# Performance work log

Measured on AMD Instinct MI355X. Metric: run time of the kernel, lower is better.

The kernel has to match this reference:

```python
import jax, jax.numpy as jnp
import numpy as np

V = 32000   # vocab
T = 256     # context len
C = 384     # n_embed
H = 6       # heads
D = 64      # head dim (HEAD_SIZE // NUM_HEADS)
L = 6       # blocks
B = 16      # batch
FF = 4 * C


def setup_inputs() -> dict:
    key = jax.random.key(0)
    ks = jax.random.split(key, 16)
    s = 0.02
    p = {}
    p["x_ids"] = jax.random.randint(ks[0], (B, T), 0, V)
    p["y_ids"] = jax.random.randint(ks[1], (B, T), 0, V)
    p["tok_emb"] = jax.random.normal(ks[2], (V, C), jnp.float32) * s
    p["pos_emb"] = jax.random.normal(ks[3], (T, C), jnp.float32) * s
    p["Wq"] = jax.random.normal(ks[4], (L, H, C, D), jnp.float32) * s
    p["Wk"] = jax.random.normal(ks[5], (L, H, C, D), jnp.float32) * s
    p["Wv"] = jax.random.normal(ks[6], (L, H, C, D), jnp.float32) * s
    p["Wo"] = jax.random.normal(ks[7], (L, H * D, C), jnp.float32) * s
    p["bo"] = jnp.zeros((L, C), jnp.float32)
    p["ln1_s"] = jnp.ones((L, C), jnp.float32)
    p["ln1_b"] = jnp.zeros((L, C), jnp.float32)
    p["ln2_s"] = jnp.ones((L, C), jnp.float32)
    p["ln2_b"] = jnp.zeros((L, C), jnp.float32)
    p["W1"] = jax.random.normal(ks[8], (L, C, FF), jnp.float32) * s
    p["b1"] = jnp.zeros((L, FF), jnp.float32)
    p["W2"] = jax.random.normal(ks[9], (L, FF, C), jnp.float32) * s
    p["b2"] = jnp.zeros((L, C), jnp.float32)
    p["lnf_s"] = jnp.ones((C,), jnp.float32)
    p["lnf_b"] = jnp.zeros((C,), jnp.float32)
    p["Whead"] = jax.random.normal(ks[10], (C, V), jnp.float32) * s
    p["bhead"] = jnp.zeros((V,), jnp.float32)
    return p


def _ln(x, scale, bias, eps=1e-5):
    m = x.mean(-1, keepdims=True)
    v = ((x - m) ** 2).mean(-1, keepdims=True)
    return (x - m) * jax.lax.rsqrt(v + eps) * scale + bias


def reference(x_ids, y_ids, tok_emb, pos_emb, Wq, Wk, Wv, Wo, bo,
              ln1_s, ln1_b, ln2_s, ln2_b, W1, b1, W2, b2,
              lnf_s, lnf_b, Whead, bhead):
    Bq, Tq = x_ids.shape
    x = tok_emb[x_ids] + pos_emb[:Tq]                      # [B,T,C]
    mask = jnp.tril(jnp.ones((Tq, Tq), bool))
    scale = C ** -0.5  # NOTE: original scales by input dim C, not head dim
    for l in range(L):
        h = _ln(x, ln1_s[l], ln1_b[l])
        q = jnp.einsum('btc,hcd->bhtd', h, Wq[l])
        k = jnp.einsum('btc,hcd->bhtd', h, Wk[l])
        v = jnp.einsum('btc,hcd->bhtd', h, Wv[l])
        att = jnp.einsum('bhtd,bhsd->bhts', q, k) * scale
        att = jnp.where(mask, att, -jnp.inf)
        att = jax.nn.softmax(att, axis=-1)
        o = jnp.einsum('bhts,bhsd->bhtd', att, v)
        o = o.transpose(0, 2, 1, 3).reshape(Bq, Tq, H * D)  # concat heads
        x = x + o @ Wo[l] + bo[l]
        h2 = _ln(x, ln2_s[l], ln2_b[l])
        x = x + jax.nn.relu(h2 @ W1[l] + b1[l]) @ W2[l] + b2[l]
    x = _ln(x, lnf_s, lnf_b)
    logits = x @ Whead + bhead                             # [B,T,V]
    logp = jax.nn.log_softmax(logits, axis=-1)
    loss = -jnp.take_along_axis(logp, y_ids[..., None], axis=-1).mean()
    return (logits, loss)
```

## Files before the change

kernel.cpp:

```cpp
#include <hip/hip_runtime.h>

typedef unsigned short u16;
typedef u16   u16x8 __attribute__((ext_vector_type(8)));
typedef short s16x8 __attribute__((ext_vector_type(8)));
typedef float f32x4 __attribute__((ext_vector_type(4)));

#define NV 32000
#define NT 256
#define NC 384
#define NH 6
#define ND 64
#define NL 6
#define NB 16
#define NFF 1536
#define NM (NB*NT)
#define QKVSZ (NB*NH*NT*ND)
#define NSLAB (NV/64)

__device__ __forceinline__ u16 f2bf(float f){
    unsigned x = __builtin_bit_cast(unsigned, f);
    x += 0x7fffu + ((x>>16)&1u);
    return (u16)(x>>16);
}

__device__ __forceinline__ void gload_lds16(const u16* g, u16* l){
    __builtin_amdgcn_global_load_lds((const __attribute__((address_space(1))) unsigned int*)g,
                                     (__attribute__((address_space(3))) unsigned int*)l, 16, 0, 0);
}

__global__ __launch_bounds__(256) void embed_kernel(const int* __restrict__ ids,
        const float* __restrict__ tok, const float* __restrict__ pos, float* __restrict__ x){
    int i4 = (blockIdx.x*256 + threadIdx.x)*4;
    int m = i4 / NC; int c = i4 - m*NC; int t = m & (NT-1);
    const float4 a = *(const float4*)(tok + (size_t)ids[m]*NC + c);
    const float4 b = *(const float4*)(pos + t*NC + c);
    *(float4*)(x + i4) = float4{a.x+b.x, a.y+b.y, a.z+b.z, a.w+b.w};
}

__global__ __launch_bounds__(256) void ln_kernel(const float* __restrict__ x,
        const float* __restrict__ sc, const float* __restrict__ bi, u16* __restrict__ out){
    int row  = blockIdx.x*4 + (threadIdx.x>>6);
    int lane = threadIdx.x & 63;
    const float* xr = x + (size_t)row*NC;
    float v[6]; float sum = 0.f, sq = 0.f;
    #pragma unroll
    for (int i=0;i<6;++i){ v[i]=xr[lane+64*i]; sum+=v[i]; sq+=v[i]*v[i]; }
    #pragma unroll
    for (int off=1; off<64; off<<=1){ sum += __shfl_xor(sum,off); sq += __shfl_xor(sq,off); }
    float mean = sum*(1.f/NC);
    float var  = sq*(1.f/NC) - mean*mean;
    float rstd = rsqrtf(var + 1e-5f);
    u16* orow = out + (size_t)row*NC;
    #pragma unroll
    for (int i=0;i<6;++i){ int c = lane+64*i; orow[c] = f2bf((v[i]-mean)*rstd*sc[c] + bi[c]); }
}

struct TDesc {
    const float* in; u16* out;
    int Cc; int nx; int perZ; int obDiv; int oStride; int start;
    long inBatch; long oS1; long oS2; float scale;
};
struct TPack { TDesc d[7]; };

__global__ __launch_bounds__(256) void tconv_all(TPack p){
    __shared__ float tile[32][33];
    int bid = blockIdx.x;
    int e = 0;
    #pragma unroll
    for (int i=1;i<7;++i) e += (bid >= p.d[i].start) ? 1 : 0;
    TDesc D = p.d[e];
    int local = bid - D.start;
    int bz  = local / D.perZ; int rem = local - bz*D.perZ;
    int cy  = rem / D.nx;     int cx  = rem - cy*D.nx;
    int r0 = cy*32, c0 = cx*32;
    const float* ib = D.in + (size_t)bz*D.inBatch;
    u16* ob = D.out + (size_t)(bz/D.obDiv)*D.oS1 + (size_t)(bz%D.obDiv)*D.oS2;
    int tx = threadIdx.x & 31, ty = threadIdx.x >> 5;
    #pragma unroll
    for (int i=0;i<4;++i) tile[ty+8*i][tx] = ib[(size_t)(r0+ty+8*i)*D.Cc + (c0+tx)];
    __syncthreads();
    #pragma unroll
    for (int i=0;i<4;++i) ob[(size_t)(c0+ty+8*i)*D.oStride + (r0+tx)] = f2bf(tile[tx][ty+8*i]*D.scale);
}

template<int EPI, int BM>
__global__ __launch_bounds__(256,2) void gemm_bt(
        const u16* __restrict__ A, const u16* __restrict__ Bt,
        const float* __restrict__ bias, float* __restrict__ resid,
        u16* __restrict__ outb, float* __restrict__ outf, float* __restrict__ lpart,
        int M, int N, int K){
    constexpr int MI = BM/32;
    __shared__ u16 As[BM*32];
    __shared__ u16 Bs[128*32];
    int tid = threadIdx.x;
    int lane = tid & 63, wid = tid >> 6;
    int wm = wid >> 1, wn = wid & 1;
    int l15 = lane & 15, lg = lane >> 4;
    int m0 = blockIdx.y * BM, n0 = blockIdx.x * 128;
    f32x4 acc[MI][4];
    #pragma unroll
    for (int a=0;a<MI;++a)
        #pragma unroll
        for (int b=0;b<4;++b) acc[a][b] = f32x4{0.f,0.f,0.f,0.f};

    int nk = K >> 5;
    for (int kk = 0; kk < nk; ++kk){
        int k0 = kk << 5;
        #pragma unroll
        for (int i=0;i<BM/64;++i){
            int o   = i*4096 + tid*16;
            int row = o >> 6;
            int kb  = (o & 63) >> 1;
            gload_lds16(A + (size_t)(m0+row)*K + (k0+kb), As + (o>>1));
        }
        #pragma unroll
        for (int i=0;i<2;++i){
            int o   = i*4096 + tid*16;
            int row = o >> 6;
            int kb  = (o & 63) >> 1;
            gload_lds16(Bt + (size_t)(n0+row)*K + (k0+kb), Bs + (o>>1));
        }
        asm volatile("s_waitcnt vmcnt(0)" ::: "memory");
        __syncthreads();
        s16x8 af[MI], bfr[4];
        #pragma unroll
        for (int mi=0;mi<MI;++mi) af[mi]  = *(const s16x8*)&As[(wm*(BM/2)+mi*16+l15)*32 + lg*8];
        #pragma unroll
        for (int ni=0;ni<4;++ni) bfr[ni] = *(const s16x8*)&Bs[(wn*64+ni*16+l15)*32 + lg*8];
        #pragma unroll
        for (int mi=0;mi<MI;++mi)
            #pragma unroll
            for (int ni=0;ni<4;++ni)
                acc[mi][ni] = __builtin_amdgcn_mfma_f32_16x16x32_bf16(af[mi], bfr[ni], acc[mi][ni], 0,0,0);
        __syncthreads();
    }

    if (EPI == 3){
        float es[MI][4];
        #pragma unroll
        for (int mi=0;mi<MI;++mi)
            #pragma unroll
            for (int r=0;r<4;++r) es[mi][r] = 0.f;
        #pragma unroll
        for (int mi=0;mi<MI;++mi)
            #pragma unroll
            for (int ni=0;ni<4;++ni)
                #pragma unroll
                for (int r=0;r<4;++r){
                    int mg = m0 + wm*(BM/2) + mi*16 + lg*4 + r;
                    int ng = n0 + wn*64 + ni*16 + l15;
                    float val = acc[mi][ni][r] + bias[ng];
                    outf[(size_t)mg*N + ng] = val;
                    es[mi][r] += __expf(val);
                }
        #pragma unroll
        for (int mi=0;mi<MI;++mi)
            #pragma unroll
            for (int r=0;r<4;++r){
                float s = es[mi][r];
                s += __shfl_xor(s,1); s += __shfl_xor(s,2);
                s += __shfl_xor(s,4); s += __shfl_xor(s,8);
                if (l15 == 0){
                    int mg = m0 + wm*(BM/2) + mi*16 + lg*4 + r;
                    lpart[(size_t)mg*NSLAB + blockIdx.x*2 + wn] = s;
                }
            }
        return;
    }

    #pragma unroll
    for (int mi=0;mi<MI;++mi){
        #pragma unroll
        for (int ni=0;ni<4;++ni){
            #pragma unroll
            for (int r=0;r<4;++r){
                int mg = m0 + wm*(BM/2) + mi*16 + lg*4 + r;
                int ng = n0 + wn*64 + ni*16 + l15;
                float c = acc[mi][ni][r];
                if (EPI == 0){
                    int which = ng / NC; int hd = ng - which*NC;
                    int hh = hd >> 6, d = hd & 63;
                    int bb = mg >> 8, tt = mg & (NT-1);
                    outb[(size_t)which*QKVSZ + ((size_t)(bb*NH+hh)*NT + tt)*ND + d] = f2bf(c);
                } else if (EPI == 1){
                    float* pp = resid + (size_t)mg*N + ng;
                    *pp = *pp + c + bias[ng];
                } else if (EPI == 2){
                    outb[(size_t)mg*N + ng] = f2bf(fmaxf(c + bias[ng], 0.f));
                }
            }
        }
    }
}

__global__ __launch_bounds__(256,2) void attn_kernel(const u16* __restrict__ qkv, u16* __restrict__ o){
    int blk = blockIdx.x;
    int qt = blk & 3, bh = blk >> 2;
    int b = bh / NH, h = bh - b*NH;
    int tid = threadIdx.x, lane = tid & 63, w = tid >> 6;
    int l15 = lane & 15, lg = lane >> 4;
    __shared__ u16 Ks[256*72];
    __shared__ u16 Vt[64*264];
    __shared__ u16 Ps[4][16*72];
    const u16* qb = qkv + (size_t)bh*NT*ND;
    const u16* kb = qb + QKVSZ;
    const u16* vb = kb + QKVSZ;
    int nit = (qt+1)*2;
    for (int it=0; it<nit; ++it){
        int idx = it*256 + tid;
        int e0 = idx*8;
        int row = e0 >> 6, col = e0 & 63;
        *(u16x8*)&Ks[row*72+col] = *(const u16x8*)(kb + e0);
        u16x8 vv = *(const u16x8*)(vb + e0);
        #pragma unroll
        for (int j=0;j<8;++j) Vt[(col+j)*264 + row] = vv[j];
    }
    const u16* qrow = qb + (size_t)(qt*64 + w*16 + l15)*ND;
    s16x8 qf[2];
    qf[0] = *(const s16x8*)(qrow + lg*8);
    qf[1] = *(const s16x8*)(qrow + 32 + lg*8);
    __syncthreads();

    f32x4 oacc[4]; float l_[4];
    #pragma unroll
    for (int c=0;c<4;++c){ oacc[c]=f32x4{0.f,0.f,0.f,0.f}; l_[c]=0.f; }
    u16* Pw = &Ps[w][0];

    for (int kt=0; kt<=qt; ++kt){
        f32x4 sacc[4];
        #pragma unroll
        for (int c=0;c<4;++c) sacc[c]=f32x4{0.f,0.f,0.f,0.f};
        #pragma unroll
        for (int ks=0;ks<2;++ks){
            s16x8 kf[4];
            #pragma unroll
            for (int ni=0;ni<4;++ni)
                kf[ni] = *(const s16x8*)&Ks[(kt*64+ni*16+l15)*72 + ks*32 + lg*8];
            #pragma unroll
            for (int ni=0;ni<4;++ni)
                sacc[ni] = __builtin_amdgcn_mfma_f32_16x16x32_bf16(qf[ks], kf[ni], sacc[ni], 0,0,0);
        }
        if (kt == qt){
            #pragma unroll
            for (int ni=0;ni<4;++ni)
                #pragma unroll
                for (int r=0;r<4;++r)
                    if (ni*16+l15 > w*16+lg*4+r) sacc[ni][r] = -1e30f;
        }
        #pragma unroll
        for (int r=0;r<4;++r){
            float rs = 0.f;
            #pragma unroll
            for (int ni=0;ni<4;++ni){
                float p = __expf(sacc[ni][r]);
                sacc[ni][r] = p;
                rs += p;
                Pw[(lg*4+r)*72 + ni*16 + l15] = f2bf(p);
            }
            rs += __shfl_xor(rs,1); rs += __shfl_xor(rs,2);
            rs += __shfl_xor(rs,4); rs += __shfl_xor(rs,8);
            l_[r] += rs;
        }
        #pragma unroll
        for (int ks=0;ks<2;++ks){
            s16x8 pf, vf[4];
            pf = *(const s16x8*)&Pw[l15*72 + ks*32 + lg*8];
            #pragma unroll
            for (int ni=0;ni<4;++ni)
                vf[ni] = *(const s16x8*)&Vt[(ni*16+l15)*264 + kt*64 + ks*32 + lg*8];
            #pragma unroll
            for (int ni=0;ni<4;++ni)
                oacc[ni] = __builtin_amdgcn_mfma_f32_16x16x32_bf16(pf, vf[ni], oacc[ni], 0,0,0);
        }
    }
    #pragma unroll
    for (int ni=0;ni<4;++ni)
        #pragma unroll
        for (int r=0;r<4;++r){
            int t = qt*64 + w*16 + lg*4 + r;
            int d = ni*16 + l15;
            o[((size_t)(b*NT + t))*NC + h*ND + d] = f2bf(oacc[ni][r] / l_[r]);
        }
}

__global__ __launch_bounds__(256) void loss_rows2(const float* __restrict__ lpart,
        const float* __restrict__ logits, const int* __restrict__ y, float* __restrict__ rowloss){
    int row  = blockIdx.x*4 + (threadIdx.x>>6);
    int lane = threadIdx.x & 63;
    const float* pr = lpart + (size_t)row*NSLAB;
    float s = 0.f;
    for (int i = lane; i < NSLAB; i += 64) s += pr[i];
    #pragma unroll
    for (int off=1; off<64; off<<=1) s += __shfl_xor(s, off);
    if (lane==0)
        rowloss[row] = logf(s) - logits[(size_t)row*NV + y[row]];
}

__global__ __launch_bounds__(256) void loss_final(const float* __restrict__ rowloss, float* __restrict__ out){
    int tid = threadIdx.x;
    float s = 0.f;
    for (int i = tid; i < NM; i += 256) s += rowloss[i];
    #pragma unroll
    for (int off=1; off<64; off<<=1) s += __shfl_xor(s, off);
    __shared__ float ss[4];
    if ((tid&63)==0) ss[tid>>6]=s;
    __syncthreads();
    if (tid==0) out[0] = (ss[0]+ss[1]+ss[2]+ss[3]) * (1.f/NM);
}

extern "C" void kernel_launch(void* const* d_in, const int* in_sizes, int n_in,
                              void* d_out, int out_size, void* d_ws, size_t ws_size,
                              hipStream_t stream){
    const int*   x_ids = (const int*)  d_in[0];
    const int*   y_ids = (const int*)  d_in[1];
    const float* tok   = (const float*)d_in[2];
    const float* pos   = (const float*)d_in[3];
    const float* Wq    = (const float*)d_in[4];
    const float* Wk    = (const float*)d_in[5];
    const float* Wv    = (const float*)d_in[6];
    const float* Wo    = (const float*)d_in[7];
    const float* bo    = (const float*)d_in[8];
    const float* ln1s  = (const float*)d_in[9];
    const float* ln1b  = (const float*)d_in[10];
    const float* ln2s  = (const float*)d_in[11];
    const float* ln2b  = (const float*)d_in[12];
    const float* W1    = (const float*)d_in[13];
    const float* b1    = (const float*)d_in[14];
    const float* W2    = (const float*)d_in[15];
    const float* b2    = (const float*)d_in[16];
    const float* lnfs  = (const float*)d_in[17];
    const float* lnfb  = (const float*)d_in[18];
    const float* Wh    = (const float*)d_in[19];
    const float* bh    = (const float*)d_in[20];

    float* logits = (float*)d_out;
    float* lossp  = logits + (size_t)NM*NV;

    char* ws = (char*)d_ws;
    auto alloc = [&](size_t bytes)->char*{ char* p = ws; ws += (bytes + 255) & ~(size_t)255; return p; };
    float* xf    = (float*)alloc((size_t)NM*NC*4);
    u16*   hbf   = (u16*)  alloc((size_t)NM*NC*2);
    u16*   qkvb  = (u16*)  alloc((size_t)3*QKVSZ*2);
    u16*   obf   = (u16*)  alloc((size_t)NM*NC*2);
    u16*   f1bf  = (u16*)  alloc((size_t)NM*NFF*2);
    u16*   qkvw  = (u16*)  alloc((size_t)NL*1152*NC*2);
    u16*   wot   = (u16*)  alloc((size_t)NL*NC*NC*2);
    u16*   w1t   = (u16*)  alloc((size_t)NL*NFF*NC*2);
    u16*   w2t   = (u16*)  alloc((size_t)NL*NC*NFF*2);
    u16*   wht   = (u16*)  alloc((size_t)NV*NC*2);
    float* part  = (float*)alloc((size_t)NM*4);
    float* lpart = (float*)qkvb;

    const float qscale = 0.051031036307982884f;

    TPack tp;
    tp.d[0] = {Wq, qkvw + 0*(NC*NC), ND,  2,  24, NH, NC, 0,     (long)NC*ND, (long)1152*NC, (long)ND*NC, qscale};
    tp.d[1] = {Wk, qkvw + 1*(NC*NC), ND,  2,  24, NH, NC, 864,   (long)NC*ND, (long)1152*NC, (long)ND*NC, 1.f};
    tp.d[2] = {Wv, qkvw + 2*(NC*NC), ND,  2,  24, NH, NC, 1728,  (long)NC*ND, (long)1152*NC, (long)ND*NC, 1.f};
    tp.d[3] = {Wo, wot,              NC, 12, 144, 1,  NC, 2592,  (long)NC*NC, (long)NC*NC,   0,           1.f};
    tp.d[4] = {W1, w1t,             NFF, 48, 576, 1,  NC, 3456,  (long)NC*NFF,(long)NFF*NC,  0,           1.f};
    tp.d[5] = {W2, w2t,              NC, 12, 576, 1, NFF, 6912,  (long)NFF*NC,(long)NC*NFF,  0,           1.f};
    tp.d[6] = {Wh, wht,              NV,1000,12000,1, NC, 10368, 0,           0,             0,           1.f};
    tconv_all<<<22368,256,0,stream>>>(tp);

    embed_kernel<<<NM*NC/1024,256,0,stream>>>(x_ids, tok, pos, xf);
    for (int l = 0; l < NL; ++l){
        ln_kernel<<<NM/4,256,0,stream>>>(xf, ln1s + l*NC, ln1b + l*NC, hbf);
        gemm_bt<0,64><<<dim3(1152/128, NM/64),256,0,stream>>>(hbf, qkvw + (size_t)l*1152*NC,
                nullptr, nullptr, qkvb, nullptr, nullptr, NM, 1152, NC);
        attn_kernel<<<NB*NH*4,256,0,stream>>>(qkvb, obf);
        gemm_bt<1,64><<<dim3(NC/128, NM/64),256,0,stream>>>(obf, wot + (size_t)l*NC*NC,
                bo + l*NC, xf, nullptr, nullptr, nullptr, NM, NC, NC);
        ln_kernel<<<NM/4,256,0,stream>>>(xf, ln2s + l*NC, ln2b + l*NC, hbf);
        gemm_bt<2,64><<<dim3(NFF/128, NM/64),256,0,stream>>>(hbf, w1t + (size_t)l*NFF*NC,
                b1 + l*NFF, nullptr, f1bf, nullptr, nullptr, NM, NFF, NC);
        gemm_bt<1,64><<<dim3(NC/128, NM/64),256,0,stream>>>(f1bf, w2t + (size_t)l*NC*NFF,
                b2 + l*NC, xf, nullptr, nullptr, nullptr, NM, NC, NFF);
    }
    ln_kernel<<<NM/4,256,0,stream>>>(xf, lnfs, lnfb, hbf);
    gemm_bt<3,128><<<dim3(NV/128, NM/128),256,0,stream>>>(hbf, wht, bh,
            nullptr, nullptr, logits, lpart, NM, NV, NC);
    loss_rows2<<<NM/4,256,0,stream>>>(lpart, logits, y_ids, part);
    loss_final<<<1,256,0,stream>>>(part, lossp);
}
```

Baseline: 836.4 us.

## Widen GEMM K-step, enlarge LM-head tile with grid swizzle, fuse embed with LN

The GEMM template gains a BN parameter and loads a K-step of 64, split into two 32-wide LDS halves, so each loop iteration runs twice as many MFMAs per barrier pair. The LM-head GEMM moves to 128x256 tiles, with a block-index swizzle that groups blocks sharing the same vocab slab to improve L2 reuse of the head weights, and NSLAB is halved to match. The embedding kernel is fused with the first layernorm, which removes one full pass over the activations. The costs are more LDS per block, which may lower occupancy, more accumulator registers in the 128x256 head GEMM, and a swizzle that hardcodes 32 M-tiles.

```diff
diff --git a/kernel.cpp b/kernel.cpp
--- a/kernel.cpp
+++ b/kernel.cpp
@@ -15,7 +15,7 @@
 #define NFF 1536
 #define NM (NB*NT)
 #define QKVSZ (NB*NH*NT*ND)
-#define NSLAB (NV/64)
+#define NSLAB (NV/128)
 
 __device__ __forceinline__ u16 f2bf(float f){
     unsigned x = __builtin_bit_cast(unsigned, f);
@@ -28,13 +28,31 @@
                                      (__attribute__((address_space(3))) unsigned int*)l, 16, 0, 0);
 }
 
-__global__ __launch_bounds__(256) void embed_kernel(const int* __restrict__ ids,
-        const float* __restrict__ tok, const float* __restrict__ pos, float* __restrict__ x){
-    int i4 = (blockIdx.x*256 + threadIdx.x)*4;
-    int m = i4 / NC; int c = i4 - m*NC; int t = m & (NT-1);
-    const float4 a = *(const float4*)(tok + (size_t)ids[m]*NC + c);
-    const float4 b = *(const float4*)(pos + t*NC + c);
-    *(float4*)(x + i4) = float4{a.x+b.x, a.y+b.y, a.z+b.z, a.w+b.w};
+__global__ __launch_bounds__(256) void embed_ln(const int* __restrict__ ids,
+        const float* __restrict__ tok, const float* __restrict__ pos,
+        const float* __restrict__ sc, const float* __restrict__ bi,
+        float* __restrict__ x, u16* __restrict__ out){
+    int row  = blockIdx.x*4 + (threadIdx.x>>6);
+    int lane = threadIdx.x & 63;
+    int t = row & (NT-1);
+    const float* tr = tok + (size_t)ids[row]*NC;
+    const float* pr = pos + (size_t)t*NC;
+    float* xr = x + (size_t)row*NC;
+    float v[6]; float sum = 0.f, sq = 0.f;
+    #pragma unroll
+    for (int i=0;i<6;++i){
+        int c = lane+64*i;
+        v[i] = tr[c] + pr[c];
+        xr[c] = v[i];
+        sum += v[i]; sq += v[i]*v[i];
+    }
+    #pragma unroll
+    for (int off=1; off<64; off<<=1){ sum += __shfl_xor(sum,off); sq += __shfl_xor(sq,off); }
+    float mean = sum*(1.f/NC);
+    float rstd = rsqrtf(sq*(1.f/NC) - mean*mean + 1e-5f);
+    u16* orow = out + (size_t)row*NC;
+    #pragma unroll
+    for (int i=0;i<6;++i){ int c = lane+64*i; orow[c] = f2bf((v[i]-mean)*rstd*sc[c] + bi[c]); }
 }
 
 __global__ __launch_bounds__(256) void ln_kernel(const float* __restrict__ x,
@@ -48,8 +66,7 @@
     #pragma unroll
     for (int off=1; off<64; off<<=1){ sum += __shfl_xor(sum,off); sq += __shfl_xor(sq,off); }
     float mean = sum*(1.f/NC);
-    float var  = sq*(1.f/NC) - mean*mean;
-    float rstd = rsqrtf(var + 1e-5f);
+    float rstd = rsqrtf(sq*(1.f/NC) - mean*mean + 1e-5f);
     u16* orow = out + (size_t)row*NC;
     #pragma unroll
     for (int i=0;i<6;++i){ int c = lane+64*i; orow[c] = f2bf((v[i]-mean)*rstd*sc[c] + bi[c]); }
@@ -83,55 +100,69 @@
     for (int i=0;i<4;++i) ob[(size_t)(c0+ty+8*i)*D.oStride + (r0+tx)] = f2bf(tile[tx][ty+8*i]*D.scale);
 }
 
-template<int EPI, int BM>
+template<int EPI, int BM, int BN, int SWZ>
 __global__ __launch_bounds__(256,2) void gemm_bt(
         const u16* __restrict__ A, const u16* __restrict__ Bt,
         const float* __restrict__ bias, float* __restrict__ resid,
         u16* __restrict__ outb, float* __restrict__ outf, float* __restrict__ lpart,
         int M, int N, int K){
-    constexpr int MI = BM/32;
-    __shared__ u16 As[BM*32];
-    __shared__ u16 Bs[128*32];
+    constexpr int WM = BM/2, WN = BN/2, MI = WM/16, NI = WN/16;
+    __shared__ u16 As[2*BM*32];
+    __shared__ u16 Bs[2*BN*32];
     int tid = threadIdx.x;
     int lane = tid & 63, wid = tid >> 6;
     int wm = wid >> 1, wn = wid & 1;
     int l15 = lane & 15, lg = lane >> 4;
-    int m0 = blockIdx.y * BM, n0 = blockIdx.x * 128;
-    f32x4 acc[MI][4];
+    int bx, by;
+    if (SWZ){
+        int nwg = gridDim.x*gridDim.y;
+        int orig = blockIdx.y*gridDim.x + blockIdx.x;
+        int swz = (orig&7)*(nwg>>3) + (orig>>3);
+        by = swz & 31;
+        bx = swz >> 5;
+    } else { bx = blockIdx.x; by = blockIdx.y; }
+    int m0 = by * BM, n0 = bx * BN;
+    f32x4 acc[MI][NI];
     #pragma unroll
     for (int a=0;a<MI;++a)
         #pragma unroll
-        for (int b=0;b<4;++b) acc[a][b] = f32x4{0.f,0.f,0.f,0.f};
-
-    int nk = K >> 5;
+        for (int b=0;b<NI;++b) acc[a][b] = f32x4{0.f,0.f,0.f,0.f};
+
+    int nk = K >> 6;
     for (int kk = 0; kk < nk; ++kk){
-        int k0 = kk << 5;
-        #pragma unroll
-        for (int i=0;i<BM/64;++i){
-            int o   = i*4096 + tid*16;
-            int row = o >> 6;
-            int kb  = (o & 63) >> 1;
-            gload_lds16(A + (size_t)(m0+row)*K + (k0+kb), As + (o>>1));
-        }
-        #pragma unroll
-        for (int i=0;i<2;++i){
-            int o   = i*4096 + tid*16;
-            int row = o >> 6;
-            int kb  = (o & 63) >> 1;
-            gload_lds16(Bt + (size_t)(n0+row)*K + (k0+kb), Bs + (o>>1));
+        int k0 = kk << 6;
+        #pragma unroll
+        for (int h=0;h<2;++h){
+            #pragma unroll
+            for (int i=0;i<BM/64;++i){
+                int o   = i*4096 + tid*16;
+                int row = o >> 6;
+                int kb  = (o & 63) >> 1;
+                gload_lds16(A + (size_t)(m0+row)*K + (k0+h*32+kb), As + h*BM*32 + (o>>1));
+            }
+            #pragma unroll
+            for (int i=0;i<BN/64;++i){
+                int o   = i*4096 + tid*16;
+                int row = o >> 6;
+                int kb  = (o & 63) >> 1;
+                gload_lds16(Bt + (size_t)(n0+row)*K + (k0+h*32+kb), Bs + h*BN*32 + (o>>1));
+            }
         }
         asm volatile("s_waitcnt vmcnt(0)" ::: "memory");
         __syncthreads();
-        s16x8 af[MI], bfr[4];
-        #pragma unroll
-        for (int mi=0;mi<MI;++mi) af[mi]  = *(const s16x8*)&As[(wm*(BM/2)+mi*16+l15)*32 + lg*8];
-        #pragma unroll
-        for (int ni=0;ni<4;++ni) bfr[ni] = *(const s16x8*)&Bs[(wn*64+ni*16+l15)*32 + lg*8];
-        #pragma unroll
-        for (int mi=0;mi<MI;++mi)
-            #pragma unroll
-            for (int ni=0;ni<4;++ni)
-                acc[mi][ni] = __builtin_amdgcn_mfma_f32_16x16x32_bf16(af[mi], bfr[ni], acc[mi][ni], 0,0,0);
+        #pragma unroll
+        for (int ks=0;ks<2;++ks){
+            s16x8 af[MI], bfr[NI];
+            #pragma unroll
+            for (int mi=0;mi<MI;++mi) af[mi]  = *(const s16x8*)&As[ks*BM*32 + (wm*WM+mi*16+l15)*32 + lg*8];
+            #pragma unroll
+            for (int ni=0;ni<NI;++ni) bfr[ni] = *(const s16x8*)&Bs[ks*BN*32 + (wn*WN+ni*16+l15)*32 + lg*8];
+            #pragma unroll
+            for (int mi=0;mi<MI;++mi)
+                #pragma unroll
+                for (int ni=0;ni<NI;++ni)
+                    acc[mi][ni] = __builtin_amdgcn_mfma_f32_16x16x32_bf16(af[mi], bfr[ni], acc[mi][ni], 0,0,0);
+        }
         __syncthreads();
     }
 
@@ -144,11 +175,11 @@
         #pragma unroll
         for (int mi=0;mi<MI;++mi)
             #pragma unroll
-            for (int ni=0;ni<4;++ni)
+            for (int ni=0;ni<NI;++ni)
                 #pragma unroll
                 for (int r=0;r<4;++r){
-                    int mg = m0 + wm*(BM/2) + mi*16 + lg*4 + r;
-                    int ng = n0 + wn*64 + ni*16 + l15;
+                    int mg = m0 + wm*WM + mi*16 + lg*4 + r;
+                    int ng = n0 + wn*WN + ni*16 + l15;
                     float val = acc[mi][ni][r] + bias[ng];
                     outf[(size_t)mg*N + ng] = val;
                     es[mi][r] += __expf(val);
@@ -161,8 +192,8 @@
                 s += __shfl_xor(s,1); s += __shfl_xor(s,2);
                 s += __shfl_xor(s,4); s += __shfl_xor(s,8);
                 if (l15 == 0){
-                    int mg = m0 + wm*(BM/2) + mi*16 + lg*4 + r;
-                    lpart[(size_t)mg*NSLAB + blockIdx.x*2 + wn] = s;
+                    int mg = m0 + wm*WM + mi*16 + lg*4 + r;
+                    lpart[(size_t)mg*NSLAB + bx*2 + wn] = s;
                 }
             }
         return;
@@ -171,11 +202,11 @@
     #pragma unroll
     for (int mi=0;mi<MI;++mi){
         #pragma unroll
-        for (int ni=0;ni<4;++ni){
+        for (int ni=0;ni<NI;++ni){
             #pragma unroll
             for (int r=0;r<4;++r){
-                int mg = m0 + wm*(BM/2) + mi*16 + lg*4 + r;
-                int ng = n0 + wn*64 + ni*16 + l15;
+                int mg = m0 + wm*WM + mi*16 + lg*4 + r;
+                int ng = n0 + wn*WN + ni*16 + l15;
                 float c = acc[mi][ni][r];
                 if (EPI == 0){
                     int which = ng / NC; int hd = ng - which*NC;
@@ -363,22 +394,24 @@
     tp.d[6] = {Wh, wht,              NV,1000,12000,1, NC, 10368, 0,           0,             0,           1.f};
     tconv_all<<<22368,256,0,stream>>>(tp);
 
-    embed_kernel<<<NM*NC/1024,256,0,stream>>>(x_ids, tok, pos, xf);
+    embed_ln<<<NM/4,256,0,stream>>>(x_ids, tok, pos, ln1s, ln1b, xf, hbf);
     for (int l = 0; l < NL; ++l){
-        ln_kernel<<<NM/4,256,0,stream>>>(xf, ln1s + l*NC, ln1b + l*NC, hbf);
-        gemm_bt<0,64><<<dim3(1152/128, NM/64),256,0,stream>>>(hbf, qkvw + (size_t)l*1152*NC,
+        gemm_bt<0,64,128,0><<<dim3(1152/128, NM/64),256,0,stream>>>(hbf, qkvw + (size_t)l*1152*NC,
                 nullptr, nullptr, qkvb, nullptr, nullptr, NM, 1152, NC);
         attn_kernel<<<NB*NH*4,256,0,stream>>>(qkvb, obf);
-        gemm_bt<1,64><<<dim3(NC/128, NM/64),256,0,stream>>>(obf, wot + (size_t)l*NC*NC,
+        gemm_bt<1,64,128,0><<<dim3(NC/128, NM/64),256,0,stream>>>(obf, wot + (size_t)l*NC*NC,
                 bo + l*NC, xf, nullptr, nullptr, nullptr, NM, NC, NC);
         ln_kernel<<<NM/4,256,0,stream>>>(xf, ln2s + l*NC, ln2b + l*NC, hbf);
-        gemm_bt<2,64><<<dim3(NFF/128, NM/64),256,0,stream>>>(hbf, w1t + (size_t)l*NFF*NC,
+        gemm_bt<2,64,128,0><<<dim3(NFF/128, NM/64),256,0,stream>>>(hbf, w1t + (size_t)l*NFF*NC,
                 b1 + l*NFF, nullptr, f1bf, nullptr, nullptr, NM, NFF, NC);
-        gemm_bt<1,64><<<dim3(NC/128, NM/64),256,0,stream>>>(f1bf, w2t + (size_t)l*NC*NFF,
+        gemm_bt<1,64,128,0><<<dim3(NC/128, NM/64),256,0,stream>>>(f1bf, w2t + (size_t)l*NC*NFF,
                 b2 + l*NC, xf, nullptr, nullptr, nullptr, NM, NC, NFF);
-    }
-    ln_kernel<<<NM/4,256,0,stream>>>(xf, lnfs, lnfb, hbf);
-    gemm_bt<3,128><<<dim3(NV/128, NM/128),256,0,stream>>>(hbf, wht, bh,
+        if (l < NL-1)
+            ln_kernel<<<NM/4,256,0,stream>>>(xf, ln1s + (l+1)*NC, ln1b + (l+1)*NC, hbf);
+        else
+            ln_kernel<<<NM/4,256,0,stream>>>(xf, lnfs, lnfb, hbf);
+    }
+    gemm_bt<3,128,256,1><<<dim3(NV/256, NM/128),256,0,stream>>>(hbf, wht, bh,
             nullptr, nullptr, logits, lpart, NM, NV, NC);
     loss_rows2<<<NM/4,256,0,stream>>>(lpart, logits, y_ids, part);
     loss_final<<<1,256,0,stream>>>(part, lossp);
```

New measurement: 850.6 us. Within noise of the previous version (+1.7%).
